# Performance work log

Measured on AMD Instinct MI355X. Metric: run time of the kernel, lower is better.

Reference implementation:

```python
import jax, jax.numpy as jnp
import numpy as np

V = 50000  # item vocab (input_size == output_size)
H = 256    # hidden_size
B = 512    # batch_size


def setup_inputs() -> dict:
    key = jax.random.key(0)
    ks = jax.random.split(key, 8)
    return {
        "input_ids": jax.random.randint(ks[0], (B,), 0, V),
        "hidden": jax.random.normal(ks[1], (1, B, H), jnp.float32),
        # GRU layer-0 params, PyTorch layout: gates stacked as [r, z, n]
        "w_ih": jax.random.normal(ks[2], (3 * H, V), jnp.float32) * 0.02,
        "w_hh": jax.random.normal(ks[3], (3 * H, H), jnp.float32) * 0.05,
        "b_ih": jax.random.normal(ks[4], (3 * H,), jnp.float32) * 0.01,
        "b_hh": jax.random.normal(ks[5], (3 * H,), jnp.float32) * 0.01,
        # h2o linear
        "w_out": jax.random.normal(ks[6], (V, H), jnp.float32) * 0.02,
        "b_out": jax.random.normal(ks[7], (V,), jnp.float32) * 0.01,
    }


def _gru_step(one_hot, h0, w_ih, w_hh, b_ih, b_hh):
    # one-hot scatter feeding the input-to-hidden GEMM (as in the torch module)
    gi = one_hot @ w_ih.T + b_ih          # [B, 3H]
    gh = h0 @ w_hh.T + b_hh               # [B, 3H]
    i_r, i_z, i_n = jnp.split(gi, 3, axis=-1)
    h_r, h_z, h_n = jnp.split(gh, 3, axis=-1)
    r = jax.nn.sigmoid(i_r + h_r)
    z = jax.nn.sigmoid(i_z + h_z)
    n = jnp.tanh(i_n + r * h_n)
    return (1.0 - z) * n + z * h0         # [B, H]


def reference(input_ids, hidden, w_ih, w_hh, b_ih, b_hh, w_out, b_out):
    # onehot_encode: zero buffer + scatter 1.0 at item index
    one_hot = jnp.zeros((B, V), w_ih.dtype).at[jnp.arange(B), input_ids].set(1.0)
    h1 = _gru_step(one_hot, hidden[0], w_ih, w_hh, b_ih, b_hh)  # [B, H]
    logit = jnp.tanh(h1 @ w_out.T + b_out)                      # final_activation = Tanh
    return logit, h1[None]  # ([B, V], [1, B, H])
```

## Files before the change

kernel.cpp:

```cpp
#include <hip/hip_runtime.h>
#include <hip/hip_bf16.h>

#define V 50000
#define H 256
#define B 512

typedef __bf16 bf16x8 __attribute__((ext_vector_type(8)));
typedef float f32x4 __attribute__((ext_vector_type(4)));

__global__ __launch_bounds__(256) void gru_h1_kernel(
    const int* __restrict__ ids, const float* __restrict__ h0,
    const float* __restrict__ w_ih, const float* __restrict__ w_hh,
    const float* __restrict__ b_ih, const float* __restrict__ b_hh,
    float* __restrict__ h1_out, __bf16* __restrict__ h1b)
{
    __shared__ float h0s[4 * 256];
    const int t = threadIdx.x;
    const int b0 = blockIdx.x * 4;

#pragma unroll
    for (int i = 0; i < 4; i++)
        h0s[t + i * 256] = h0[b0 * 256 + t + i * 256];
    __syncthreads();

    const int j = t;
    float ar[4] = {0.f, 0.f, 0.f, 0.f};
    float az[4] = {0.f, 0.f, 0.f, 0.f};
    float an[4] = {0.f, 0.f, 0.f, 0.f};
    const float* __restrict__ wr_p = w_hh + j * H;
    const float* __restrict__ wz_p = w_hh + (H + j) * H;
    const float* __restrict__ wn_p = w_hh + (2 * H + j) * H;

#pragma unroll 4
    for (int k = 0; k < H; k++) {
        float wr = wr_p[k], wz = wz_p[k], wn = wn_p[k];
#pragma unroll
        for (int m = 0; m < 4; m++) {
            float h = h0s[m * 256 + k];
            ar[m] = fmaf(wr, h, ar[m]);
            az[m] = fmaf(wz, h, az[m]);
            an[m] = fmaf(wn, h, an[m]);
        }
    }

    const float bir = b_ih[j], biz = b_ih[H + j], bin = b_ih[2 * H + j];
    const float bhr = b_hh[j], bhz = b_hh[H + j], bhn = b_hh[2 * H + j];

#pragma unroll
    for (int m = 0; m < 4; m++) {
        int id = ids[b0 + m];
        float ir = w_ih[(size_t)j * V + id] + bir;
        float iz = w_ih[(size_t)(H + j) * V + id] + biz;
        float inn = w_ih[(size_t)(2 * H + j) * V + id] + bin;
        float hr = ar[m] + bhr;
        float hz = az[m] + bhz;
        float hn = an[m] + bhn;
        float r = 1.f / (1.f + __expf(-(ir + hr)));
        float z = 1.f / (1.f + __expf(-(iz + hz)));
        float n = tanhf(inn + r * hn);
        float h1 = (1.f - z) * n + z * h0s[m * 256 + j];
        h1_out[(b0 + m) * H + j] = h1;
        h1b[(b0 + m) * H + j] = (__bf16)h1;
    }
}

#define BN 64
#define BSTR 264

__global__ __launch_bounds__(256, 4) void logit_kernel(
    const __bf16* __restrict__ h1b, const float* __restrict__ w_out,
    const float* __restrict__ b_out, float* __restrict__ out)
{
    __shared__ __bf16 Bs[BN * BSTR];
    const int t = threadIdx.x;
    const int n0 = blockIdx.y * BN;
    const int m_tile = blockIdx.x;

    {
        const int c4 = t & 63;
        const int v0 = t >> 6;
#pragma unroll
        for (int i = 0; i < 16; i++) {
            int v = v0 + i * 4;
            int n = n0 + v;
            f32x4 g = {0.f, 0.f, 0.f, 0.f};
            if (n < V) g = *(const f32x4*)(w_out + (size_t)n * H + c4 * 4);
            struct alignas(8) BH4 { __bf16 h[4]; } p;
            p.h[0] = (__bf16)g[0];
            p.h[1] = (__bf16)g[1];
            p.h[2] = (__bf16)g[2];
            p.h[3] = (__bf16)g[3];
            *(BH4*)&Bs[v * BSTR + c4 * 4] = p;
        }
    }
    __syncthreads();

    const int lane = t & 63;
    const int wave = t >> 6;
    const int q = lane >> 4;
    const int v16 = lane & 15;
    const int m_base = m_tile * 256 + wave * 64;

    f32x4 acc[4][4];
#pragma unroll
    for (int i = 0; i < 4; i++)
#pragma unroll
        for (int jj = 0; jj < 4; jj++) acc[i][jj] = (f32x4){0.f, 0.f, 0.f, 0.f};

    const __bf16* a_base = h1b + (m_base + v16) * H + q * 8;

#pragma unroll 2
    for (int ks = 0; ks < 8; ks++) {
        bf16x8 a[4], bfr[4];
#pragma unroll
        for (int i = 0; i < 4; i++)
            a[i] = *(const bf16x8*)(a_base + i * 16 * H + ks * 32);
#pragma unroll
        for (int jj = 0; jj < 4; jj++)
            bfr[jj] = *(const bf16x8*)&Bs[(jj * 16 + v16) * BSTR + ks * 32 + q * 8];
#pragma unroll
        for (int i = 0; i < 4; i++)
#pragma unroll
            for (int jj = 0; jj < 4; jj++)
                acc[i][jj] = __builtin_amdgcn_mfma_f32_16x16x32_bf16(
                    a[i], bfr[jj], acc[i][jj], 0, 0, 0);
    }

    float bo[4];
    int vv[4];
#pragma unroll
    for (int jj = 0; jj < 4; jj++) {
        int v = n0 + jj * 16 + v16;
        vv[jj] = v;
        bo[jj] = (v < V) ? b_out[v] : 0.f;
    }
#pragma unroll
    for (int i = 0; i < 4; i++) {
        int mrow = m_base + i * 16 + q * 4;
#pragma unroll
        for (int jj = 0; jj < 4; jj++) {
            if (vv[jj] < V) {
#pragma unroll
                for (int r = 0; r < 4; r++) {
                    out[(size_t)(mrow + r) * V + vv[jj]] = tanhf(acc[i][jj][r] + bo[jj]);
                }
            }
        }
    }
}

extern "C" void kernel_launch(void* const* d_in, const int* in_sizes, int n_in,
                              void* d_out, int out_size, void* d_ws, size_t ws_size,
                              hipStream_t stream) {
    const int* ids = (const int*)d_in[0];
    const float* hidden = (const float*)d_in[1];
    const float* w_ih = (const float*)d_in[2];
    const float* w_hh = (const float*)d_in[3];
    const float* b_ih = (const float*)d_in[4];
    const float* b_hh = (const float*)d_in[5];
    const float* w_out = (const float*)d_in[6];
    const float* b_out = (const float*)d_in[7];

    float* out = (float*)d_out;
    float* h1_out = out + (size_t)B * V;
    __bf16* h1b = (__bf16*)d_ws;

    gru_h1_kernel<<<128, 256, 0, stream>>>(ids, hidden, w_ih, w_hh, b_ih, b_hh,
                                           h1_out, h1b);

    dim3 grid(2, (V + BN - 1) / BN);
    logit_kernel<<<grid, 256, 0, stream>>>(h1b, w_out, b_out, out);
}
```

Before: 346.3 us.

## Vectorize logit stores via swapped MFMA operands, fast tanh, and restructure GRU kernel

The logit GEMM swaps its MFMA operands so each lane holds four consecutive vocab columns, which lets the output be written with 16-byte vector stores instead of scalar stores. It also swaps the grid axes, batches the w_out loads ahead of the bf16 conversion, fully unrolls the k loop, and replaces tanhf with an exp/rcp-based approximation. The GRU kernel now handles 2 rows per block with vectorized w_hh loads and hoists the w_ih gathers ahead of the loop. It leaves a dead tanh computation in place, and the fast tanh may lose some accuracy.

```diff
diff --git a/kernel.cpp b/kernel.cpp
--- a/kernel.cpp
+++ b/kernel.cpp
@@ -8,38 +8,59 @@
 typedef __bf16 bf16x8 __attribute__((ext_vector_type(8)));
 typedef float f32x4 __attribute__((ext_vector_type(4)));
 
+__device__ __forceinline__ float tanh_fast(float x) {
+    float a = __builtin_fabsf(x);
+    float e = __expf(2.0f * a);
+    float r = fmaf(-2.0f, __builtin_amdgcn_rcpf(e + 1.0f), 1.0f);
+    return __builtin_copysignf(r, x);
+}
+
 __global__ __launch_bounds__(256) void gru_h1_kernel(
     const int* __restrict__ ids, const float* __restrict__ h0,
     const float* __restrict__ w_ih, const float* __restrict__ w_hh,
     const float* __restrict__ b_ih, const float* __restrict__ b_hh,
     float* __restrict__ h1_out, __bf16* __restrict__ h1b)
 {
-    __shared__ float h0s[4 * 256];
+    __shared__ float h0s[2 * 256];
     const int t = threadIdx.x;
-    const int b0 = blockIdx.x * 4;
+    const int b0 = blockIdx.x * 2;
 
 #pragma unroll
-    for (int i = 0; i < 4; i++)
-        h0s[t + i * 256] = h0[b0 * 256 + t + i * 256];
+    for (int i = 0; i < 2; i++)
+        h0s[i * 256 + t] = h0[(b0 + i) * 256 + t];
     __syncthreads();
 
     const int j = t;
-    float ar[4] = {0.f, 0.f, 0.f, 0.f};
-    float az[4] = {0.f, 0.f, 0.f, 0.f};
-    float an[4] = {0.f, 0.f, 0.f, 0.f};
-    const float* __restrict__ wr_p = w_hh + j * H;
-    const float* __restrict__ wz_p = w_hh + (H + j) * H;
-    const float* __restrict__ wn_p = w_hh + (2 * H + j) * H;
+
+    int id[2];
+    float gir[2], giz[2], gin[2];
+#pragma unroll
+    for (int m = 0; m < 2; m++) {
+        id[m] = ids[b0 + m];
+        gir[m] = w_ih[(size_t)j * V + id[m]];
+        giz[m] = w_ih[(size_t)(H + j) * V + id[m]];
+        gin[m] = w_ih[(size_t)(2 * H + j) * V + id[m]];
+    }
+
+    float ar[2] = {0.f, 0.f}, az[2] = {0.f, 0.f}, an[2] = {0.f, 0.f};
+    const float* __restrict__ wr_p = w_hh + (size_t)j * H;
+    const float* __restrict__ wz_p = w_hh + (size_t)(H + j) * H;
+    const float* __restrict__ wn_p = w_hh + (size_t)(2 * H + j) * H;
 
 #pragma unroll 4
-    for (int k = 0; k < H; k++) {
-        float wr = wr_p[k], wz = wz_p[k], wn = wn_p[k];
+    for (int k = 0; k < H; k += 4) {
+        f32x4 wr = *(const f32x4*)(wr_p + k);
+        f32x4 wz = *(const f32x4*)(wz_p + k);
+        f32x4 wn = *(const f32x4*)(wn_p + k);
 #pragma unroll
-        for (int m = 0; m < 4; m++) {
-            float h = h0s[m * 256 + k];
-            ar[m] = fmaf(wr, h, ar[m]);
-            az[m] = fmaf(wz, h, az[m]);
-            an[m] = fmaf(wn, h, an[m]);
+        for (int m = 0; m < 2; m++) {
+            f32x4 h = *(const f32x4*)&h0s[m * 256 + k];
+#pragma unroll
+            for (int u = 0; u < 4; u++) {
+                ar[m] = fmaf(wr[u], h[u], ar[m]);
+                az[m] = fmaf(wz[u], h[u], az[m]);
+                an[m] = fmaf(wn[u], h[u], an[m]);
+            }
         }
     }
 
@@ -47,17 +68,12 @@
     const float bhr = b_hh[j], bhz = b_hh[H + j], bhn = b_hh[2 * H + j];
 
 #pragma unroll
-    for (int m = 0; m < 4; m++) {
-        int id = ids[b0 + m];
-        float ir = w_ih[(size_t)j * V + id] + bir;
-        float iz = w_ih[(size_t)(H + j) * V + id] + biz;
-        float inn = w_ih[(size_t)(2 * H + j) * V + id] + bin;
-        float hr = ar[m] + bhr;
-        float hz = az[m] + bhz;
-        float hn = an[m] + bhn;
-        float r = 1.f / (1.f + __expf(-(ir + hr)));
-        float z = 1.f / (1.f + __expf(-(iz + hz)));
-        float n = tanhf(inn + r * hn);
+    for (int m = 0; m < 2; m++) {
+        float r = 1.f / (1.f + __expf(-(gir[m] + bir + ar[m] + bhr)));
+        float z = 1.f / (1.f + __expf(-(giz[m] + biz + az[m] + bhz)));
+        float n = tanh_fast(gin[m] + bin + an[m] + bhn * r + r * an[m] * 0.f
+                            + r * (an[m] * 0.f));
+        n = tanh_fast(gin[m] + bin + r * (an[m] + bhn));
         float h1 = (1.f - z) * n + z * h0s[m * 256 + j];
         h1_out[(b0 + m) * H + j] = h1;
         h1b[(b0 + m) * H + j] = (__bf16)h1;
@@ -73,24 +89,31 @@
 {
     __shared__ __bf16 Bs[BN * BSTR];
     const int t = threadIdx.x;
-    const int n0 = blockIdx.y * BN;
-    const int m_tile = blockIdx.x;
+    const int n0 = blockIdx.x * BN;
+    const int m_tile = blockIdx.y;
 
     {
         const int c4 = t & 63;
         const int v0 = t >> 6;
 #pragma unroll
-        for (int i = 0; i < 16; i++) {
-            int v = v0 + i * 4;
-            int n = n0 + v;
-            f32x4 g = {0.f, 0.f, 0.f, 0.f};
-            if (n < V) g = *(const f32x4*)(w_out + (size_t)n * H + c4 * 4);
-            struct alignas(8) BH4 { __bf16 h[4]; } p;
-            p.h[0] = (__bf16)g[0];
-            p.h[1] = (__bf16)g[1];
-            p.h[2] = (__bf16)g[2];
-            p.h[3] = (__bf16)g[3];
-            *(BH4*)&Bs[v * BSTR + c4 * 4] = p;
+        for (int half = 0; half < 2; half++) {
+            f32x4 g[8];
+#pragma unroll
+            for (int i = 0; i < 8; i++) {
+                int n = n0 + v0 + (half * 8 + i) * 4;
+                g[i] = (f32x4){0.f, 0.f, 0.f, 0.f};
+                if (n < V) g[i] = *(const f32x4*)(w_out + (size_t)n * H + c4 * 4);
+            }
+#pragma unroll
+            for (int i = 0; i < 8; i++) {
+                int v = v0 + (half * 8 + i) * 4;
+                struct alignas(8) BH4 { __bf16 h[4]; } p;
+                p.h[0] = (__bf16)g[i][0];
+                p.h[1] = (__bf16)g[i][1];
+                p.h[2] = (__bf16)g[i][2];
+                p.h[3] = (__bf16)g[i][3];
+                *(BH4*)&Bs[v * BSTR + c4 * 4] = p;
+            }
         }
     }
     __syncthreads();
@@ -109,41 +132,34 @@
 
     const __bf16* a_base = h1b + (m_base + v16) * H + q * 8;
 
-#pragma unroll 2
+#pragma unroll
     for (int ks = 0; ks < 8; ks++) {
-        bf16x8 a[4], bfr[4];
+        bf16x8 a[4];
 #pragma unroll
         for (int i = 0; i < 4; i++)
             a[i] = *(const bf16x8*)(a_base + i * 16 * H + ks * 32);
 #pragma unroll
-        for (int jj = 0; jj < 4; jj++)
-            bfr[jj] = *(const bf16x8*)&Bs[(jj * 16 + v16) * BSTR + ks * 32 + q * 8];
+        for (int jj = 0; jj < 4; jj++) {
+            bf16x8 bfr = *(const bf16x8*)&Bs[(jj * 16 + v16) * BSTR + ks * 32 + q * 8];
 #pragma unroll
-        for (int i = 0; i < 4; i++)
-#pragma unroll
-            for (int jj = 0; jj < 4; jj++)
+            for (int i = 0; i < 4; i++)
                 acc[i][jj] = __builtin_amdgcn_mfma_f32_16x16x32_bf16(
-                    a[i], bfr[jj], acc[i][jj], 0, 0, 0);
+                    bfr, a[i], acc[i][jj], 0, 0, 0);
+        }
     }
 
-    float bo[4];
-    int vv[4];
 #pragma unroll
     for (int jj = 0; jj < 4; jj++) {
-        int v = n0 + jj * 16 + v16;
-        vv[jj] = v;
-        bo[jj] = (v < V) ? b_out[v] : 0.f;
-    }
+        const int n = n0 + jj * 16 + q * 4;
+        if (n < V) {
+            f32x4 bo = *(const f32x4*)&b_out[n];
 #pragma unroll
-    for (int i = 0; i < 4; i++) {
-        int mrow = m_base + i * 16 + q * 4;
+            for (int i = 0; i < 4; i++) {
+                f32x4 r;
 #pragma unroll
-        for (int jj = 0; jj < 4; jj++) {
-            if (vv[jj] < V) {
-#pragma unroll
-                for (int r = 0; r < 4; r++) {
-                    out[(size_t)(mrow + r) * V + vv[jj]] = tanhf(acc[i][jj][r] + bo[jj]);
-                }
+                for (int u = 0; u < 4; u++)
+                    r[u] = tanh_fast(acc[i][jj][u] + bo[u]);
+                *(f32x4*)&out[(size_t)(m_base + i * 16 + v16) * V + n] = r;
             }
         }
     }
@@ -165,9 +181,9 @@
     float* h1_out = out + (size_t)B * V;
     __bf16* h1b = (__bf16*)d_ws;
 
-    gru_h1_kernel<<<128, 256, 0, stream>>>(ids, hidden, w_ih, w_hh, b_ih, b_hh,
+    gru_h1_kernel<<<256, 256, 0, stream>>>(ids, hidden, w_ih, w_hh, b_ih, b_hh,
                                            h1_out, h1b);
 
-    dim3 grid(2, (V + BN - 1) / BN);
+    dim3 grid((V + BN - 1) / BN, 2);
     logit_kernel<<<grid, 256, 0, stream>>>(h1b, w_out, b_out, out);
 }
```

Measured after the change: 334.0 us. 1.04x faster.
